# Optimization experiments

Hardware: AMD Instinct MI355X
Metric: run time of the kernel (lower is better)

Reference implementation:

```python
import jax, jax.numpy as jnp
import numpy as np

N, B, L, E = 64, 128, 4096, 16
BN_EPS = 1e-5


def setup_inputs() -> dict:
    key = jax.random.key(0)
    ks = jax.random.split(key, 6)
    feat = jax.random.normal(ks[0], (N, B, L), dtype=jnp.float32)
    # Glorot-ish scaled linear weights
    Wl = jax.random.normal(ks[1], (L, E), dtype=jnp.float32) * (1.0 / np.sqrt(L))
    Wr = jax.random.normal(ks[2], (L, E), dtype=jnp.float32) * (1.0 / np.sqrt(L))
    Wm = jax.random.normal(ks[3], (L, L), dtype=jnp.float32) * (1.0 / np.sqrt(L))
    return {
        "feat": feat,
        "Wl": Wl, "bl": jnp.zeros((E,), jnp.float32),
        "Wr": Wr, "br": jnp.zeros((E,), jnp.float32),
        "Wm": Wm, "bm": jnp.zeros((L,), jnp.float32),
        "gamma": jnp.ones((N * N,), jnp.float32),
        "beta": jnp.zeros((N * N,), jnp.float32),
        "bias": jnp.zeros((L,), jnp.float32),
    }


def reference(feat, Wl, bl, Wr, br, Wm, bm, gamma, beta, bias):
    # feat: (N, B, L) node time series
    # Attention projections (lookup_l / lookup_r): Linear(L -> E)
    att_l = feat @ Wl + bl                      # (N, B, E) on src nodes
    att_r = feat @ Wr + br                      # (N, B, E) on dst nodes

    # Feature extractor: MLP Linear(L, L) + ReLU over the time axis
    out = jax.nn.relu(jnp.einsum('nbl,kl->nbk', feat, Wm) + bm)   # (N, B, L)

    # Edge scores on the complete graph: e[d, s, b] = att_l[src=s] . att_r[dst=d]
    e = jnp.einsum('sbe,dbe->dsb', att_l, att_r)                  # (Nd, Ns, B)

    # BatchNorm1d over N*N edge channels (training-mode batch statistics)
    ef = e.reshape(N * N, B)
    mu = ef.mean(axis=1, keepdims=True)
    var = ef.var(axis=1, keepdims=True)
    ef = gamma[:, None] * (ef - mu) * jax.lax.rsqrt(var + BN_EPS) + beta[:, None]
    e = ef.reshape(N, N, B)

    # edge_softmax: normalize over incoming edges (src axis) per destination node
    w = jax.nn.softmax(e, axis=1)                                  # (Nd, Ns, B)

    # Weighted neighbor aggregation + bias
    rst = jnp.einsum('dsb,sbl->dbl', w, out) + bias                # (N, B, L)
    return rst
```

## Files before the change

### kernel.cpp

```cpp
#include <hip/hip_runtime.h>
#include <stdint.h>
#include <stddef.h>

#define NN 64
#define BB 128
#define LL 4096
#define EE 16

typedef __attribute__((ext_vector_type(4))) float f32x4;
typedef __attribute__((ext_vector_type(8))) short short8;
typedef __attribute__((ext_vector_type(4))) unsigned short u16x4;

__device__ __forceinline__ unsigned short f2bf(float f) {
  union { float f; unsigned u; } v; v.f = f;
  unsigned r = v.u + 0x7FFFu + ((v.u >> 16) & 1u);
  return (unsigned short)(r >> 16);
}
__device__ __forceinline__ float bf2f(unsigned short h) {
  union { unsigned u; float f; } v; v.u = ((unsigned)h) << 16;
  return v.f;
}
__device__ __forceinline__ void gload16(const void* g, void* l) {
  __builtin_amdgcn_global_load_lds((const __attribute__((address_space(1))) void*)g,
                                   (__attribute__((address_space(3))) void*)l,
                                   16, 0, 0);
}

__global__ __launch_bounds__(256) void k_cvt(const float* __restrict__ src,
                                             unsigned short* __restrict__ dst, int n4) {
  int i = blockIdx.x * 256 + threadIdx.x;
  int stride = gridDim.x * 256;
  for (; i < n4; i += stride) {
    f32x4 v = ((const f32x4*)src)[i];
    u16x4 o;
    o[0] = f2bf(v[0]); o[1] = f2bf(v[1]); o[2] = f2bf(v[2]); o[3] = f2bf(v[3]);
    ((u16x4*)dst)[i] = o;
  }
}

__global__ __launch_bounds__(256) void k_att(const float* __restrict__ feat,
    const float* __restrict__ Wl, const float* __restrict__ bl,
    const float* __restrict__ Wr, const float* __restrict__ br,
    unsigned short* __restrict__ feat_bf,
    float* __restrict__ att_l, float* __restrict__ att_r) {
  __shared__ __align__(16) float wlds[128][36];
  __shared__ __align__(16) float flds[8][132];
  __shared__ __align__(16) float red[4][64][4];
  int t = threadIdx.x;
  int rowBase = blockIdx.x * 8;
  int lane = t & 63, wave = t >> 6;
  int row = lane >> 3, eg = lane & 7;
  float acc0 = 0.f, acc1 = 0.f, acc2 = 0.f, acc3 = 0.f;
  for (int kc = 0; kc < 32; ++kc) {
    int k0 = kc * 128;
    __syncthreads();
    for (int i = t; i < 512; i += 256) {
      int kk = i >> 2, ee = (i & 3) * 4;
      *(f32x4*)&wlds[kk][ee]      = *(const f32x4*)&Wl[(size_t)(k0 + kk) * 16 + ee];
      *(f32x4*)&wlds[kk][16 + ee] = *(const f32x4*)&Wr[(size_t)(k0 + kk) * 16 + ee];
    }
    {
      int rr = t >> 5, kk = (t & 31) * 4;
      size_t gi = (size_t)(rowBase + rr) * LL + k0 + kk;
      f32x4 v = *(const f32x4*)&feat[gi];
      *(f32x4*)&flds[rr][kk] = v;
      u16x4 o; o[0] = f2bf(v[0]); o[1] = f2bf(v[1]); o[2] = f2bf(v[2]); o[3] = f2bf(v[3]);
      *(u16x4*)&feat_bf[gi] = o;
    }
    __syncthreads();
    int kb = wave * 32;
    #pragma unroll
    for (int k2 = 0; k2 < 32; ++k2) {
      int k = kb + k2;
      float fv = flds[row][k];
      f32x4 wv = *(const f32x4*)&wlds[k][eg * 4];
      acc0 += fv * wv[0]; acc1 += fv * wv[1]; acc2 += fv * wv[2]; acc3 += fv * wv[3];
    }
  }
  red[wave][lane][0] = acc0; red[wave][lane][1] = acc1;
  red[wave][lane][2] = acc2; red[wave][lane][3] = acc3;
  __syncthreads();
  if (t < 64) {
    f32x4 s = *(f32x4*)&red[0][t][0];
    #pragma unroll
    for (int w2 = 1; w2 < 4; ++w2) {
      f32x4 v = *(f32x4*)&red[w2][t][0];
      s[0] += v[0]; s[1] += v[1]; s[2] += v[2]; s[3] += v[3];
    }
    int r = rowBase + (t >> 3);
    int e0 = (t & 7) * 4;
    #pragma unroll
    for (int q = 0; q < 4; ++q) {
      int e = e0 + q;
      if (e < 16) att_l[(size_t)r * 16 + e]        = s[q] + bl[e];
      else        att_r[(size_t)r * 16 + (e - 16)] = s[q] + br[e - 16];
    }
  }
}

__global__ __launch_bounds__(256) void k_edge(const float* __restrict__ att_l,
    const float* __restrict__ att_r, const float* __restrict__ gamma,
    const float* __restrict__ beta, float* __restrict__ w_t) {
  __shared__ __align__(16) float attr[BB][20];
  __shared__ float el[NN][BB + 1];
  __shared__ float part[NN][4][2];
  __shared__ float sc[NN], sh[NN];
  int d = blockIdx.x, t = threadIdx.x;
  for (int i = t; i < 512; i += 256) {
    int b = i >> 2, e = (i & 3) * 4;
    *(f32x4*)&attr[b][e] = *(const f32x4*)&att_r[((size_t)d * BB + b) * 16 + e];
  }
  __syncthreads();
  for (int v = t; v < NN * BB; v += 256) {
    int s = v >> 7, b = v & 127;
    const float* al = &att_l[((size_t)s * BB + b) * 16];
    float acc = 0.f;
    #pragma unroll
    for (int e4 = 0; e4 < 4; ++e4) {
      f32x4 a = *(const f32x4*)&al[e4 * 4];
      f32x4 r = *(const f32x4*)&attr[b][e4 * 4];
      acc += a[0] * r[0] + a[1] * r[1] + a[2] * r[2] + a[3] * r[3];
    }
    el[s][b] = acc;
  }
  __syncthreads();
  {
    int s = t >> 2, q = t & 3;
    float sum = 0.f, ss = 0.f;
    for (int b = q * 32; b < q * 32 + 32; ++b) { float x = el[s][b]; sum += x; ss += x * x; }
    part[s][q][0] = sum; part[s][q][1] = ss;
  }
  __syncthreads();
  if (t < 64) {
    float sum = 0.f, ss = 0.f;
    #pragma unroll
    for (int q = 0; q < 4; ++q) { sum += part[t][q][0]; ss += part[t][q][1]; }
    float mu = sum * (1.f / 128.f);
    float var = ss * (1.f / 128.f) - mu * mu;
    int c = d * 64 + t;
    float a = gamma[c] * rsqrtf(fmaxf(var, 0.f) + 1e-5f);
    sc[t] = a; sh[t] = beta[c] - mu * a;
  }
  __syncthreads();
  if (t < 128) {
    int b = t;
    float y[64];
    float m = -1e30f;
    #pragma unroll
    for (int s = 0; s < 64; ++s) { y[s] = sc[s] * el[s][b] + sh[s]; m = fmaxf(m, y[s]); }
    float sum = 0.f;
    #pragma unroll
    for (int s = 0; s < 64; ++s) { y[s] = __expf(y[s] - m); sum += y[s]; }
    float inv = 1.f / sum;
    float* wp = &w_t[((size_t)b * 64 + d) * 64];
    #pragma unroll
    for (int s4 = 0; s4 < 16; ++s4) {
      f32x4 o;
      o[0] = y[s4 * 4 + 0] * inv; o[1] = y[s4 * 4 + 1] * inv;
      o[2] = y[s4 * 4 + 2] * inv; o[3] = y[s4 * 4 + 3] * inv;
      *(f32x4*)&wp[s4 * 4] = o;
    }
  }
}

__global__ __launch_bounds__(256) void k_gemm(const unsigned short* __restrict__ A,
    const unsigned short* __restrict__ Bm, const float* __restrict__ bm,
    unsigned short* __restrict__ C) {
  __shared__ __align__(16) unsigned short As[128 * 32];
  __shared__ __align__(16) unsigned short Bs[128 * 32];
  int t = threadIdx.x;
  int bid = blockIdx.x;
  int tM = bid >> 5, tN = bid & 31;
  size_t rowBase = (size_t)tM * 128, colBase = (size_t)tN * 128;
  int lane = t & 63, wave = t >> 6;
  int wm = wave >> 1, wn = wave & 1;
  int srow = t >> 2, scol = (t & 3) * 8;
  const unsigned short* aP = A + (rowBase + srow) * LL + scol;
  const unsigned short* bP = Bm + (colBase + srow) * LL + scol;
  unsigned short* asD0 = As + t * 8;
  unsigned short* asD1 = As + 2048 + t * 8;
  unsigned short* bsD0 = Bs + t * 8;
  unsigned short* bsD1 = Bs + 2048 + t * 8;
  f32x4 acc[4][4] = {};
  int fro = lane & 15, fko = (lane >> 4) * 8;
  int aOff = (wm * 64 + fro) * 32 + fko;
  int bOff = (wn * 64 + fro) * 32 + fko;
  for (int kt = 0; kt < 128; ++kt) {
    int k0 = kt * 32;
    gload16(aP + k0, asD0);
    gload16(aP + (size_t)64 * LL + k0, asD1);
    gload16(bP + k0, bsD0);
    gload16(bP + (size_t)64 * LL + k0, bsD1);
    __syncthreads();
    short8 af[4], bf[4];
    #pragma unroll
    for (int mi = 0; mi < 4; ++mi) af[mi] = *(const short8*)&As[aOff + mi * 16 * 32];
    #pragma unroll
    for (int ni = 0; ni < 4; ++ni) bf[ni] = *(const short8*)&Bs[bOff + ni * 16 * 32];
    #pragma unroll
    for (int mi = 0; mi < 4; ++mi) {
      #pragma unroll
      for (int ni = 0; ni < 4; ++ni)
        acc[mi][ni] = __builtin_amdgcn_mfma_f32_16x16x32_bf16(af[mi], bf[ni], acc[mi][ni], 0, 0, 0);
    }
    __syncthreads();
  }
  int ro = (lane >> 4) * 4, co = lane & 15;
  #pragma unroll
  for (int ni = 0; ni < 4; ++ni) {
    size_t c = colBase + wn * 64 + ni * 16 + co;
    float bc = bm[c];
    #pragma unroll
    for (int mi = 0; mi < 4; ++mi) {
      size_t r0 = rowBase + wm * 64 + mi * 16 + ro;
      #pragma unroll
      for (int j = 0; j < 4; ++j) {
        float v = acc[mi][ni][j] + bc;
        v = fmaxf(v, 0.f);
        C[(r0 + j) * LL + c] = f2bf(v);
      }
    }
  }
}

__global__ __launch_bounds__(256) void k_agg(const float* __restrict__ w_t,
    const unsigned short* __restrict__ outb, const float* __restrict__ bias,
    float* __restrict__ rst) {
  __shared__ __align__(16) float wl[64][64];
  int b = blockIdx.y;
  int t = threadIdx.x;
  int l = blockIdx.x * 256 + t;
  {
    const f32x4* src = (const f32x4*)&w_t[(size_t)b * 4096];
    f32x4* dstp = (f32x4*)&wl[0][0];
    for (int i = t; i < 1024; i += 256) dstp[i] = src[i];
  }
  __syncthreads();
  float o[64];
  #pragma unroll
  for (int s = 0; s < 64; ++s) o[s] = bf2f(outb[((size_t)s * BB + b) * LL + l]);
  float bs = bias[l];
  #pragma unroll 2
  for (int d = 0; d < 64; ++d) {
    float acc = 0.f;
    #pragma unroll
    for (int s4 = 0; s4 < 16; ++s4) {
      f32x4 wv = *(const f32x4*)&wl[d][s4 * 4];
      acc += wv[0] * o[s4 * 4 + 0] + wv[1] * o[s4 * 4 + 1]
           + wv[2] * o[s4 * 4 + 2] + wv[3] * o[s4 * 4 + 3];
    }
    rst[((size_t)d * BB + b) * LL + l] = acc + bs;
  }
}

extern "C" void kernel_launch(void* const* d_in, const int* in_sizes, int n_in,
                              void* d_out, int out_size, void* d_ws, size_t ws_size,
                              hipStream_t stream) {
  (void)in_sizes; (void)n_in; (void)out_size; (void)ws_size;
  const float* feat  = (const float*)d_in[0];
  const float* Wl    = (const float*)d_in[1];
  const float* bl    = (const float*)d_in[2];
  const float* Wr    = (const float*)d_in[3];
  const float* br    = (const float*)d_in[4];
  const float* Wm    = (const float*)d_in[5];
  const float* bm    = (const float*)d_in[6];
  const float* gamma = (const float*)d_in[7];
  const float* beta  = (const float*)d_in[8];
  const float* bias  = (const float*)d_in[9];
  char* ws = (char*)d_ws;
  unsigned short* feat_bf = (unsigned short*)(ws);
  unsigned short* wm_bf   = (unsigned short*)(ws + 67108864ull);
  unsigned short* out_bf  = (unsigned short*)(ws + 100663296ull);
  float* att_l = (float*)(ws + 167772160ull);
  float* att_r = (float*)(ws + 168296448ull);
  float* w_t   = (float*)(ws + 168820736ull);
  float* rst = (float*)d_out;

  k_cvt<<<dim3(2048), dim3(256), 0, stream>>>(Wm, wm_bf, (LL * LL) / 4);
  k_att<<<dim3(1024), dim3(256), 0, stream>>>(feat, Wl, bl, Wr, br, feat_bf, att_l, att_r);
  k_edge<<<dim3(64), dim3(256), 0, stream>>>(att_l, att_r, gamma, beta, w_t);
  k_gemm<<<dim3(2048), dim3(256), 0, stream>>>(feat_bf, wm_bf, bm, out_bf);
  k_agg<<<dim3(16, 128), dim3(256), 0, stream>>>(w_t, out_bf, bias, rst);
}
```

Measured before the change: 545.5 us.

## Replace bf16 GEMM with 256x256 tiled, multi-stage pipelined 8-wave kernel

Rewrites the main MLP GEMM as an 8-wave 256x256 tile kernel with 128KB LDS holding double-buffered 64-wide K chunks. Global-to-LDS loads are prefetched ahead and interleaved with MFMA phases using explicit waitcnt and barriers. It also adds an XOR swizzle against LDS bank conflicts, s_setprio around MFMA bursts, and a block-index swizzle for L2 locality. The aim is to hide memory latency and raise data reuse per tile, at the cost of high register and LDS pressure and fragile manual synchronisation.

New measurement: 442.2 us. 1.23x faster.

```diff
diff --git a/kernel.cpp b/kernel.cpp
--- a/kernel.cpp
+++ b/kernel.cpp
@@ -163,59 +163,122 @@
   }
 }
 
-__global__ __launch_bounds__(256) void k_gemm(const unsigned short* __restrict__ A,
+#define LDS_A 0
+#define LDS_B 65536
+#define BAR   do { __builtin_amdgcn_sched_barrier(0); __builtin_amdgcn_s_barrier(); __builtin_amdgcn_sched_barrier(0); } while (0)
+#define LGKM0 do { asm volatile("s_waitcnt lgkmcnt(0)" ::: "memory"); __builtin_amdgcn_sched_barrier(0); } while (0)
+#define VM6   asm volatile("s_waitcnt vmcnt(6)" ::: "memory")
+#define VM4   asm volatile("s_waitcnt vmcnt(4)" ::: "memory")
+#define VM0   asm volatile("s_waitcnt vmcnt(0)" ::: "memory")
+#define PRIO1 __builtin_amdgcn_s_setprio(1)
+#define PRIO0 __builtin_amdgcn_s_setprio(0)
+#define MFMA(a, b, c) __builtin_amdgcn_mfma_f32_16x16x32_bf16((a), (b), (c), 0, 0, 0)
+#define STAGE2(g0, g1, ldsoff) do { \
+    gload16((g0), lds_raw + (ldsoff) + tid16); \
+    gload16((g1), lds_raw + (ldsoff) + 8192 + tid16); } while (0)
+
+__global__ __launch_bounds__(512, 2) void k_gemm8(const unsigned short* __restrict__ A,
     const unsigned short* __restrict__ Bm, const float* __restrict__ bm,
     unsigned short* __restrict__ C) {
-  __shared__ __align__(16) unsigned short As[128 * 32];
-  __shared__ __align__(16) unsigned short Bs[128 * 32];
-  int t = threadIdx.x;
+  __shared__ __align__(16) char lds_raw[131072];
+  const int tid = threadIdx.x;
+  const int lane = tid & 63, wave = tid >> 6;
+  const int wm = wave >> 2, wn = wave & 3;
   int bid = blockIdx.x;
-  int tM = bid >> 5, tN = bid & 31;
-  size_t rowBase = (size_t)tM * 128, colBase = (size_t)tN * 128;
-  int lane = t & 63, wave = t >> 6;
-  int wm = wave >> 1, wn = wave & 1;
-  int srow = t >> 2, scol = (t & 3) * 8;
-  const unsigned short* aP = A + (rowBase + srow) * LL + scol;
-  const unsigned short* bP = Bm + (colBase + srow) * LL + scol;
-  unsigned short* asD0 = As + t * 8;
-  unsigned short* asD1 = As + 2048 + t * 8;
-  unsigned short* bsD0 = Bs + t * 8;
-  unsigned short* bsD1 = Bs + 2048 + t * 8;
-  f32x4 acc[4][4] = {};
-  int fro = lane & 15, fko = (lane >> 4) * 8;
-  int aOff = (wm * 64 + fro) * 32 + fko;
-  int bOff = (wn * 64 + fro) * 32 + fko;
-  for (int kt = 0; kt < 128; ++kt) {
-    int k0 = kt * 32;
-    gload16(aP + k0, asD0);
-    gload16(aP + (size_t)64 * LL + k0, asD1);
-    gload16(bP + k0, bsD0);
-    gload16(bP + (size_t)64 * LL + k0, bsD1);
-    __syncthreads();
-    short8 af[4], bf[4];
-    #pragma unroll
-    for (int mi = 0; mi < 4; ++mi) af[mi] = *(const short8*)&As[aOff + mi * 16 * 32];
-    #pragma unroll
-    for (int ni = 0; ni < 4; ++ni) bf[ni] = *(const short8*)&Bs[bOff + ni * 16 * 32];
-    #pragma unroll
-    for (int mi = 0; mi < 4; ++mi) {
-      #pragma unroll
-      for (int ni = 0; ni < 4; ++ni)
-        acc[mi][ni] = __builtin_amdgcn_mfma_f32_16x16x32_bf16(af[mi], bf[ni], acc[mi][ni], 0, 0, 0);
-    }
-    __syncthreads();
-  }
-  int ro = (lane >> 4) * 4, co = lane & 15;
+  int swz = (bid & 7) * 64 + (bid >> 3);
+  int tM = swz >> 4, tN = swz & 15;
+  const size_t rowBase = (size_t)tM * 256, colBase = (size_t)tN * 256;
+  const int tid16 = tid * 16;
+  const int o0 = tid16, o1 = tid16 + 8192;
+  const int r0s = (o0 & 1023) >> 6, r1s = (o1 & 1023) >> 6;
+  const int row0 = (o0 >> 10) * 16 + r0s, row1 = (o1 >> 10) * 16 + r1s;
+  const int col0 = (((o0 >> 4) & 3) ^ ((r0s >> 3) << 1)) * 8;
+  const int col1 = (((o1 >> 4) & 3) ^ ((r1s >> 3) << 1)) * 8;
+  const unsigned short* aR0 = A  + (rowBase + row0) * LL + col0;
+  const unsigned short* aR1 = A  + (rowBase + row1) * LL + col1;
+  const unsigned short* bR0 = Bm + (colBase + row0) * LL + col0;
+  const unsigned short* bR1 = Bm + (colBase + row1) * LL + col1;
+  const int rr = lane & 15, gg = lane >> 4;
+  const int rdswz = rr * 64 + ((gg ^ ((rr >> 3) << 1)) << 4);
+  f32x4 acc[8][4] = {};
+  STAGE2(aR0 +  0, aR1 +  0, LDS_A + 0);
+  STAGE2(bR0 +  0, bR1 +  0, LDS_B + 0);
+  STAGE2(aR0 + 32, aR1 + 32, LDS_A + 16384);
+  STAGE2(bR0 + 32, bR1 + 32, LDS_B + 16384);
+  VM4;
+  STAGE2(aR0 + 64, aR1 + 64, LDS_A + 32768);
+  STAGE2(bR0 + 64, bR1 + 64, LDS_B + 32768);
+  STAGE2(aR0 + 96, aR1 + 96, LDS_A + 32768 + 16384);
+  VM6;
+  BAR;
+  #pragma unroll 2
+  for (int t = 0; t < 64; ++t) {
+    const int d = t & 1;
+    const char* pA = lds_raw + LDS_A + d * 32768 + wm * 8192 + rdswz;
+    const char* pB = lds_raw + LDS_B + d * 32768 + wn * 4096 + rdswz;
+    short8 ar[8], bx, by;
+    #pragma unroll
+    for (int mi = 0; mi < 8; ++mi) ar[mi] = *(const short8*)(pA + mi * 1024);
+    bx = *(const short8*)(pB + 0);
+    by = *(const short8*)(pB + 1024);
+    if (t <= 62) { size_t kc = (size_t)(t + 1) * 64 + 32;
+      STAGE2(bR0 + kc, bR1 + kc, LDS_B + ((t + 1) & 1) * 32768 + 16384); }
+    BAR; LGKM0; PRIO1;
+    #pragma unroll
+    for (int mi = 0; mi < 8; ++mi) {
+      acc[mi][0] = MFMA(ar[mi], bx, acc[mi][0]);
+      acc[mi][1] = MFMA(ar[mi], by, acc[mi][1]);
+    }
+    PRIO0; BAR;
+    bx = *(const short8*)(pB + 2048);
+    by = *(const short8*)(pB + 3072);
+    if (t <= 61) { size_t kc = (size_t)(t + 2) * 64;
+      STAGE2(aR0 + kc, aR1 + kc, LDS_A + d * 32768); }
+    BAR; LGKM0; PRIO1;
+    #pragma unroll
+    for (int mi = 0; mi < 8; ++mi) {
+      acc[mi][2] = MFMA(ar[mi], bx, acc[mi][2]);
+      acc[mi][3] = MFMA(ar[mi], by, acc[mi][3]);
+    }
+    PRIO0; BAR;
+    #pragma unroll
+    for (int mi = 0; mi < 8; ++mi) ar[mi] = *(const short8*)(pA + 16384 + mi * 1024);
+    bx = *(const short8*)(pB + 16384 + 2048);
+    by = *(const short8*)(pB + 16384 + 3072);
+    if (t <= 61) { size_t kc = (size_t)(t + 2) * 64;
+      STAGE2(bR0 + kc, bR1 + kc, LDS_B + d * 32768); }
+    BAR; LGKM0; PRIO1;
+    #pragma unroll
+    for (int mi = 0; mi < 8; ++mi) {
+      acc[mi][2] = MFMA(ar[mi], bx, acc[mi][2]);
+      acc[mi][3] = MFMA(ar[mi], by, acc[mi][3]);
+    }
+    PRIO0; BAR;
+    bx = *(const short8*)(pB + 16384);
+    by = *(const short8*)(pB + 16384 + 1024);
+    if (t <= 61) { size_t kc = (size_t)(t + 2) * 64 + 32;
+      STAGE2(aR0 + kc, aR1 + kc, LDS_A + d * 32768 + 16384); }
+    BAR; LGKM0; PRIO1;
+    #pragma unroll
+    for (int mi = 0; mi < 8; ++mi) {
+      acc[mi][0] = MFMA(ar[mi], bx, acc[mi][0]);
+      acc[mi][1] = MFMA(ar[mi], by, acc[mi][1]);
+    }
+    PRIO0;
+    if (t < 62) { VM6; } else { VM0; }
+    BAR;
+  }
+  const int co = lane & 15, ro4 = (lane >> 4) * 4;
   #pragma unroll
-  for (int ni = 0; ni < 4; ++ni) {
-    size_t c = colBase + wn * 64 + ni * 16 + co;
-    float bc = bm[c];
-    #pragma unroll
-    for (int mi = 0; mi < 4; ++mi) {
-      size_t r0 = rowBase + wm * 64 + mi * 16 + ro;
+  for (int mig = 0; mig < 8; ++mig) {
+    size_t r0 = rowBase + (size_t)wm * 128 + mig * 16 + ro4;
+    #pragma unroll
+    for (int nj = 0; nj < 4; ++nj) {
+      size_t c = colBase + (size_t)wn * 64 + nj * 16 + co;
+      float bc = bm[c];
       #pragma unroll
       for (int j = 0; j < 4; ++j) {
-        float v = acc[mi][ni][j] + bc;
+        float v = acc[mig][nj][j] + bc;
         v = fmaxf(v, 0.f);
         C[(r0 + j) * LL + c] = f2bf(v);
       }
@@ -279,6 +342,6 @@
   k_cvt<<<dim3(2048), dim3(256), 0, stream>>>(Wm, wm_bf, (LL * LL) / 4);
   k_att<<<dim3(1024), dim3(256), 0, stream>>>(feat, Wl, bl, Wr, br, feat_bf, att_l, att_r);
   k_edge<<<dim3(64), dim3(256), 0, stream>>>(att_l, att_r, gamma, beta, w_t);
-  k_gemm<<<dim3(2048), dim3(256), 0, stream>>>(feat_bf, wm_bf, bm, out_bf);
+  k_gemm8<<<dim3(512), dim3(512), 0, stream>>>(feat_bf, wm_bf, bm, out_bf);
   k_agg<<<dim3(16, 128), dim3(256), 0, stream>>>(w_t, out_bf, bias, rst);
 }
```
